# Optimization experiments

Measured on AMD Instinct MI355X. Metric: run time of the kernel, lower is better.

The kernel has to match this reference:

```python
import jax, jax.numpy as jnp
import numpy as np

N_NODES = 100000
N_EDGES = 3200000
D_IN = 256
D_OUT = 256


def setup_inputs() -> dict:
    key = jax.random.key(0)
    k1, k2, k3, k4, k5 = jax.random.split(key, 5)
    x = jax.random.normal(k1, (N_NODES, D_IN), dtype=jnp.float32)
    edge_val = jax.random.uniform(k2, (N_EDGES,), dtype=jnp.float32)
    weight = jax.random.normal(k3, (D_IN, D_OUT), dtype=jnp.float32)
    bias = jnp.zeros((D_OUT,), dtype=jnp.float32)
    edge_row = jax.random.randint(k4, (N_EDGES,), 0, N_NODES, dtype=jnp.int32)
    edge_col = jax.random.randint(k5, (N_EDGES,), 0, N_NODES, dtype=jnp.int32)
    return {"x": x, "edge_val": edge_val, "weight": weight, "bias": bias,
            "edge_row": edge_row, "edge_col": edge_col}


def reference(x, edge_val, weight, bias, edge_row, edge_col):
    # Dense feature transform: support = x @ W  -> [N, D_OUT]
    support = x @ weight
    # SpMM with COO adjacency: out[i] = sum_{e: row[e]=i} val[e] * support[col[e]]
    messages = edge_val[:, None] * support[edge_col]        # [E, D_OUT] gather
    out = jax.ops.segment_sum(messages, edge_row, num_segments=N_NODES)
    return out + bias
```

## Files before the change

kernel.cpp:

```cpp
#include <hip/hip_runtime.h>

#define D 256
#define BSHIFT 7
#define BROWS 128
#define CHUNK 8192

typedef __attribute__((ext_vector_type(8))) short bf16x8;
typedef __attribute__((ext_vector_type(4))) float f32x4;

__device__ inline ushort f2bf_rne(float f) {
    uint u = __builtin_bit_cast(uint, f);
    return (ushort)((u + 0x7FFFu + ((u >> 16) & 1u)) >> 16);
}

__global__ __launch_bounds__(256) void prep(const float* __restrict__ w,
                                            ushort* __restrict__ wt,
                                            int* __restrict__ bcnt, int NB) {
    const int idx = blockIdx.x * 256 + threadIdx.x;
    if (idx < D * D) {
        const int n = idx >> 8, k = idx & 255;
        wt[n * 256 + k] = f2bf_rne(w[k * 256 + n]);
    } else if (idx - D * D < NB) {
        bcnt[idx - D * D] = 0;
    }
}

__global__ __launch_bounds__(256) void bucket_hist(const int* __restrict__ edge_row,
                                                   int* __restrict__ bcnt,
                                                   int E, int NB) {
    __shared__ int bh[1024];
    const int tid = threadIdx.x;
    for (int i = tid; i < 1024; i += 256) bh[i] = 0;
    __syncthreads();

    const int e0 = blockIdx.x * CHUNK;
    const int e1 = min(e0 + CHUNK, E);
    for (int i = e0 + tid * 4; i < e1; i += 1024) {
        if (i + 3 < e1) {
            const int4 r = *(const int4*)(edge_row + i);
            atomicAdd(&bh[r.x >> BSHIFT], 1);
            atomicAdd(&bh[r.y >> BSHIFT], 1);
            atomicAdd(&bh[r.z >> BSHIFT], 1);
            atomicAdd(&bh[r.w >> BSHIFT], 1);
        } else {
            for (int j = i; j < e1; ++j) atomicAdd(&bh[edge_row[j] >> BSHIFT], 1);
        }
    }
    __syncthreads();

    for (int b = tid; b < NB; b += 256) {
        const int c = bh[b];
        if (c) atomicAdd(&bcnt[b], c);
    }
}

__global__ __launch_bounds__(512) void bucket_scan(const int* __restrict__ bcnt,
                                                   int* __restrict__ bstart,
                                                   int* __restrict__ bcursor,
                                                   int* __restrict__ row_start,
                                                   int NB, int N, int E) {
    __shared__ int psum[512];
    const int tid = threadIdx.x;
    int v[4];
    int s = 0;
#pragma unroll
    for (int k = 0; k < 4; ++k) {
        const int i = tid * 4 + k;
        v[k] = (i < NB) ? bcnt[i] : 0;
        s += v[k];
    }
    psum[tid] = s;
    __syncthreads();
#pragma unroll
    for (int off = 1; off < 512; off <<= 1) {
        const int t = (tid >= off) ? psum[tid - off] : 0;
        __syncthreads();
        psum[tid] += t;
        __syncthreads();
    }
    int run = psum[tid] - s;
#pragma unroll
    for (int k = 0; k < 4; ++k) {
        const int i = tid * 4 + k;
        if (i < NB) { bstart[i] = run; bcursor[i] = run; }
        run += v[k];
    }
    if (tid == 0) { bstart[NB] = E; row_start[N] = E; }
}

union SMemGS {
    ushort As[64 * 256];
    int    cur[1024];
};

__global__ __launch_bounds__(256) void gemm_scatter(
        const float* __restrict__ x, const ushort* __restrict__ wt,
        ushort* __restrict__ sup, int N, int ngemm,
        const int* __restrict__ edge_row, const int* __restrict__ edge_col,
        const float* __restrict__ edge_val, int* __restrict__ bcursor,
        unsigned long long* __restrict__ ebuck, int E, int NB, int nchunk) {
    __shared__ SMemGS sm;
    const int tid = threadIdx.x;
    const int bid = blockIdx.x;

    const bool is_scatter = ((bid % 5) == 4) && (bid / 5 < nchunk);

    if (!is_scatter) {
        const int gb = bid - (bid + 1) / 5;
        if (gb >= ngemm) return;
        const int wv  = tid >> 6;
        const int ln  = tid & 63;
        const int row0 = gb * 64;

        for (int i = tid; i < 64 * 64; i += 256) {
            const int r = i >> 6, c = i & 63;
            int gr = row0 + r;
            if (gr >= N) gr = N - 1;
            const float4 xv = *(const float4*)(x + (size_t)gr * D + c * 4);
            ushort4 b;
            b.x = f2bf_rne(xv.x); b.y = f2bf_rne(xv.y);
            b.z = f2bf_rne(xv.z); b.w = f2bf_rne(xv.w);
            const int byte = (r * 512 + c * 8) ^ ((r & 7) << 4);
            *(ushort4*)((char*)sm.As + byte) = b;
        }
        __syncthreads();

        f32x4 acc[16];
#pragma unroll
        for (int n = 0; n < 16; ++n) acc[n] = (f32x4){0.f, 0.f, 0.f, 0.f};

        const int arow = wv * 16 + (ln & 15);
        const int ksub = (ln >> 4) * 16;
        const ushort* wbase = wt + (ln & 15) * 256;

#pragma unroll
        for (int kk = 0; kk < 8; ++kk) {
            const int abyte = (arow * 512 + kk * 64 + ksub) ^ ((arow & 7) << 4);
            const bf16x8 af = *(const bf16x8*)((const char*)sm.As + abyte);
            const ushort* wp = wbase + kk * 32 + (ln >> 4) * 8;
#pragma unroll
            for (int n = 0; n < 16; ++n) {
                const bf16x8 bf = *(const bf16x8*)(wp + n * 16 * 256);
                acc[n] = __builtin_amdgcn_mfma_f32_16x16x32_bf16(af, bf, acc[n], 0, 0, 0);
            }
        }

        const int crow = row0 + wv * 16 + (ln >> 4) * 4;
        const int ccol = ln & 15;
#pragma unroll
        for (int n = 0; n < 16; ++n) {
#pragma unroll
            for (int reg = 0; reg < 4; ++reg) {
                const int r = crow + reg;
                if (r < N) sup[(size_t)r * D + n * 16 + ccol] = f2bf_rne(acc[n][reg]);
            }
        }
    } else {
        const int e0 = (bid / 5) * CHUNK;
        const int e1 = min(e0 + CHUNK, E);

        for (int i = tid; i < 1024; i += 256) sm.cur[i] = 0;
        __syncthreads();

        for (int e = e0 + tid; e < e1; e += 256)
            atomicAdd(&sm.cur[edge_row[e] >> BSHIFT], 1);
        __syncthreads();

        for (int b = tid; b < NB; b += 256) {
            const int c = sm.cur[b];
            sm.cur[b] = (c > 0) ? atomicAdd(&bcursor[b], c) : 0;
        }
        __syncthreads();

        for (int e = e0 + tid; e < e1; e += 256) {
            const int r = edge_row[e];
            const int b = r >> BSHIFT;
            const int pos = atomicAdd(&sm.cur[b], 1);
            const unsigned long long pk =
                ((unsigned long long)(uint)f2bf_rne(edge_val[e]) << 48) |
                ((unsigned long long)(uint)edge_col[e] << 17) | (uint)r;
            ebuck[pos] = pk;
        }
    }
}

__device__ inline long long pack_cv(int c, float v) {
    return (long long)(((unsigned long long)__builtin_bit_cast(uint, v) << 32) |
                       (uint)c);
}

__global__ __launch_bounds__(256) void fine_scatter(
        const unsigned long long* __restrict__ ebuck,
        const int* __restrict__ bstart,
        long long* __restrict__ epair,
        int* __restrict__ row_start, int N) {
    __shared__ int cnt[BROWS];
    __shared__ int cur[BROWS];
    const int tid = threadIdx.x;
    const int r0  = blockIdx.x << BSHIFT;
    const int s   = bstart[blockIdx.x];
    const int e   = bstart[blockIdx.x + 1];

    if (tid < BROWS) cnt[tid] = 0;
    __syncthreads();

    for (int i = s + tid; i < e; i += 256)
        atomicAdd(&cnt[(int)(ebuck[i] & 0x1FFFFu) - r0], 1);
    __syncthreads();

    if (tid < BROWS) cur[tid] = cnt[tid];
    __syncthreads();
#pragma unroll
    for (int off = 1; off < BROWS; off <<= 1) {
        const int t = (tid < BROWS && tid >= off) ? cur[tid - off] : 0;
        __syncthreads();
        if (tid < BROWS) cur[tid] += t;
        __syncthreads();
    }
    if (tid < BROWS) {
        const int rs = s + cur[tid] - cnt[tid];
        cur[tid] = rs;
        const int row = r0 + tid;
        if (row < N) row_start[row] = rs;
    }
    __syncthreads();

    for (int i = s + tid; i < e; i += 256) {
        const unsigned long long pk = ebuck[i];
        const int  r  = (int)(pk & 0x1FFFFu) - r0;
        const int  c  = (int)((pk >> 17) & 0x1FFFFu);
        const float v = __builtin_bit_cast(float, (uint)(pk >> 48) << 16);
        const int pos = atomicAdd(&cur[r], 1);
        epair[pos] = pack_cv(c, v);
    }
}

__global__ __launch_bounds__(256) void accumulate(const ushort* __restrict__ sup,
                                                  const int* __restrict__ row_start,
                                                  const long long* __restrict__ epair,
                                                  const float* __restrict__ bias,
                                                  float* __restrict__ out, int N) {
    const int row = blockIdx.x * 4 + (threadIdx.x >> 6);
    if (row >= N) return;
    const int lane = threadIdx.x & 63;
    const int lofs = lane * 4;

    const int s = row_start[row];
    const int e = row_start[row + 1];

    f32x4 a[8];
    a[0] = *(const f32x4*)(bias + lofs);
#pragma unroll
    for (int q = 1; q < 8; ++q) a[q] = (f32x4){0.f, 0.f, 0.f, 0.f};

    for (int base = s; base < e; base += 64) {
        const int idx = base + lane;
        long long pk = 0;
        if (idx < e) pk = __builtin_nontemporal_load(epair + idx);
        const int   c = (int)(uint)pk;
        const float v = __builtin_bit_cast(float, (uint)((unsigned long long)pk >> 32));
        const int n = min(64, e - base);
        int j = 0;
        for (; j + 15 < n; j += 16) {
            int   cq[16];
            float vq[16];
            uint2 uq[16];
#pragma unroll
            for (int q = 0; q < 16; ++q) {
                cq[q] = __shfl(c, j + q);
                vq[q] = __shfl(v, j + q);
            }
#pragma unroll
            for (int q = 0; q < 16; ++q)
                uq[q] = *(const uint2*)(sup + ((uint)cq[q] << 8) + lofs);
#pragma unroll
            for (int q = 0; q < 16; ++q) {
                const float f0 = __builtin_bit_cast(float, uq[q].x << 16);
                const float f1 = __builtin_bit_cast(float, uq[q].x & 0xFFFF0000u);
                const float f2 = __builtin_bit_cast(float, uq[q].y << 16);
                const float f3 = __builtin_bit_cast(float, uq[q].y & 0xFFFF0000u);
                a[q & 7][0] = fmaf(vq[q], f0, a[q & 7][0]);
                a[q & 7][1] = fmaf(vq[q], f1, a[q & 7][1]);
                a[q & 7][2] = fmaf(vq[q], f2, a[q & 7][2]);
                a[q & 7][3] = fmaf(vq[q], f3, a[q & 7][3]);
            }
        }
        for (; j + 7 < n; j += 8) {
            int   cq[8];
            float vq[8];
            uint2 uq[8];
#pragma unroll
            for (int q = 0; q < 8; ++q) {
                cq[q] = __shfl(c, j + q);
                vq[q] = __shfl(v, j + q);
            }
#pragma unroll
            for (int q = 0; q < 8; ++q)
                uq[q] = *(const uint2*)(sup + ((uint)cq[q] << 8) + lofs);
#pragma unroll
            for (int q = 0; q < 8; ++q) {
                const float f0 = __builtin_bit_cast(float, uq[q].x << 16);
                const float f1 = __builtin_bit_cast(float, uq[q].x & 0xFFFF0000u);
                const float f2 = __builtin_bit_cast(float, uq[q].y << 16);
                const float f3 = __builtin_bit_cast(float, uq[q].y & 0xFFFF0000u);
                a[q][0] = fmaf(vq[q], f0, a[q][0]);
                a[q][1] = fmaf(vq[q], f1, a[q][1]);
                a[q][2] = fmaf(vq[q], f2, a[q][2]);
                a[q][3] = fmaf(vq[q], f3, a[q][3]);
            }
        }
        for (; j < n; ++j) {
            const int   c0 = __shfl(c, j);
            const float v0 = __shfl(v, j);
            const uint2 u  = *(const uint2*)(sup + ((uint)c0 << 8) + lofs);
            const float f0 = __builtin_bit_cast(float, u.x << 16);
            const float f1 = __builtin_bit_cast(float, u.x & 0xFFFF0000u);
            const float f2 = __builtin_bit_cast(float, u.y << 16);
            const float f3 = __builtin_bit_cast(float, u.y & 0xFFFF0000u);
            a[0][0] = fmaf(v0, f0, a[0][0]);
            a[0][1] = fmaf(v0, f1, a[0][1]);
            a[0][2] = fmaf(v0, f2, a[0][2]);
            a[0][3] = fmaf(v0, f3, a[0][3]);
        }
    }
#pragma unroll
    for (int q = 1; q < 8; ++q) {
        a[0][0] += a[q][0]; a[0][1] += a[q][1];
        a[0][2] += a[q][2]; a[0][3] += a[q][3];
    }
    __builtin_nontemporal_store(a[0], (f32x4*)(out + (size_t)row * D + lofs));
}

extern "C" void kernel_launch(void* const* d_in, const int* in_sizes, int n_in,
                              void* d_out, int out_size, void* d_ws, size_t ws_size,
                              hipStream_t stream) {
    const float* x        = (const float*)d_in[0];
    const float* edge_val = (const float*)d_in[1];
    const float* weight   = (const float*)d_in[2];
    const float* bias     = (const float*)d_in[3];
    const int*   edge_row = (const int*)d_in[4];
    const int*   edge_col = (const int*)d_in[5];
    float*       out      = (float*)d_out;

    const int N = in_sizes[0] / D;
    const int E = in_sizes[1];

    char* ws = (char*)d_ws;
    size_t off = 0;
    auto carve = [&](size_t bytes) -> char* {
        char* p = ws + off;
        off = (off + bytes + 255) & ~(size_t)255;
        return p;
    };

    const int NB = (N + BROWS - 1) / BROWS;

    ushort* sup = (ushort*)carve((size_t)N * D * sizeof(ushort));
    ushort* wt  = (ushort*)carve((size_t)D * D * sizeof(ushort));
    unsigned long long* ebuck =
        (unsigned long long*)carve((size_t)E * sizeof(unsigned long long));
    long long* epair = (long long*)carve((size_t)E * sizeof(long long));
    int* row_start = (int*)carve((size_t)(N + 1) * sizeof(int));
    int* bcnt      = (int*)carve((size_t)NB * sizeof(int));
    int* bstart    = (int*)carve((size_t)(NB + 1) * sizeof(int));
    int* bcursor   = (int*)carve((size_t)NB * sizeof(int));

    const int ngemm  = (N + 63) / 64;
    const int nchunk = (E + CHUNK - 1) / CHUNK;
    const int ngrid = 5 * nchunk;

    prep<<<(D * D + NB + 255) / 256, 256, 0, stream>>>(weight, wt, bcnt, NB);

    bucket_hist<<<nchunk, 256, 0, stream>>>(edge_row, bcnt, E, NB);
    bucket_scan<<<1, 512, 0, stream>>>(bcnt, bstart, bcursor, row_start, NB, N, E);

    gemm_scatter<<<ngrid, 256, 0, stream>>>(
        x, wt, sup, N, ngemm, edge_row, edge_col, edge_val, bcursor, ebuck, E, NB,
        nchunk);

    fine_scatter<<<NB, 256, 0, stream>>>(ebuck, bstart, epair, row_start, N);

    accumulate<<<(N + 3) / 4, 256, 0, stream>>>(sup, row_start, epair, bias, out, N);
}
```

Measured before the change: 400.3 us.

## Fuse fine bucket sort with row accumulation and halve bucket size

The per-bucket fine scatter and the per-row gather-accumulate are merged into one kernel. Each block first sorts its bucket's edges by row in a scratch buffer, then its four waves accumulate that bucket's rows straight from the just-written pairs. Buckets shrink from 128 to 64 rows, doubling the histogram and scatter shared arrays, and the global row_start array plus one kernel launch go away. The intent is to cut a launch and keep the epair reads hot in cache. The cost is fewer, heavier blocks (one per 64 rows) with a barrier between the two phases, which may lower latency hiding and add load imbalance.

```diff
diff --git a/kernel.cpp b/kernel.cpp
--- a/kernel.cpp
+++ b/kernel.cpp
@@ -1,8 +1,8 @@
 #include <hip/hip_runtime.h>
 
 #define D 256
-#define BSHIFT 7
-#define BROWS 128
+#define BSHIFT 6
+#define BROWS 64
 #define CHUNK 8192
 
 typedef __attribute__((ext_vector_type(8))) short bf16x8;
@@ -28,9 +28,9 @@
 __global__ __launch_bounds__(256) void bucket_hist(const int* __restrict__ edge_row,
                                                    int* __restrict__ bcnt,
                                                    int E, int NB) {
-    __shared__ int bh[1024];
+    __shared__ int bh[2048];
     const int tid = threadIdx.x;
-    for (int i = tid; i < 1024; i += 256) bh[i] = 0;
+    for (int i = tid; i < 2048; i += 256) bh[i] = 0;
     __syncthreads();
 
     const int e0 = blockIdx.x * CHUNK;
@@ -57,8 +57,7 @@
 __global__ __launch_bounds__(512) void bucket_scan(const int* __restrict__ bcnt,
                                                    int* __restrict__ bstart,
                                                    int* __restrict__ bcursor,
-                                                   int* __restrict__ row_start,
-                                                   int NB, int N, int E) {
+                                                   int NB, int E) {
     __shared__ int psum[512];
     const int tid = threadIdx.x;
     int v[4];
@@ -85,12 +84,12 @@
         if (i < NB) { bstart[i] = run; bcursor[i] = run; }
         run += v[k];
     }
-    if (tid == 0) { bstart[NB] = E; row_start[N] = E; }
+    if (tid == 0) bstart[NB] = E;
 }
 
 union SMemGS {
     ushort As[64 * 256];
-    int    cur[1024];
+    int    cur[2048];
 };
 
 __global__ __launch_bounds__(256) void gemm_scatter(
@@ -159,7 +158,7 @@
         const int e0 = (bid / 5) * CHUNK;
         const int e1 = min(e0 + CHUNK, E);
 
-        for (int i = tid; i < 1024; i += 256) sm.cur[i] = 0;
+        for (int i = tid; i < 2048; i += 256) sm.cur[i] = 0;
         __syncthreads();
 
         for (int e = e0 + tid; e < e1; e += 256)
@@ -189,17 +188,23 @@
                        (uint)c);
 }
 
-__global__ __launch_bounds__(256) void fine_scatter(
+__global__ __launch_bounds__(256) void sort_accumulate(
+        const ushort* __restrict__ sup,
         const unsigned long long* __restrict__ ebuck,
         const int* __restrict__ bstart,
         long long* __restrict__ epair,
-        int* __restrict__ row_start, int N) {
+        const float* __restrict__ bias,
+        float* __restrict__ out, int N) {
     __shared__ int cnt[BROWS];
     __shared__ int cur[BROWS];
-    const int tid = threadIdx.x;
-    const int r0  = blockIdx.x << BSHIFT;
-    const int s   = bstart[blockIdx.x];
-    const int e   = bstart[blockIdx.x + 1];
+    __shared__ int srow[BROWS + 1];
+    const int tid  = threadIdx.x;
+    const int lane = tid & 63;
+    const int wv   = tid >> 6;
+    const int r0   = blockIdx.x << BSHIFT;
+    const int s    = bstart[blockIdx.x];
+    const int e    = bstart[blockIdx.x + 1];
+    const int lofs = lane * 4;
 
     if (tid < BROWS) cnt[tid] = 0;
     __syncthreads();
@@ -218,11 +223,11 @@
         __syncthreads();
     }
     if (tid < BROWS) {
-        const int rs = s + cur[tid] - cnt[tid];
-        cur[tid] = rs;
-        const int row = r0 + tid;
-        if (row < N) row_start[row] = rs;
-    }
+        const int ex = cur[tid] - cnt[tid];
+        srow[tid] = ex;
+        cur[tid]  = s + ex;
+    }
+    if (tid == 0) srow[BROWS] = e - s;
     __syncthreads();
 
     for (int i = s + tid; i < e; i += 256) {
@@ -233,102 +238,96 @@
         const int pos = atomicAdd(&cur[r], 1);
         epair[pos] = pack_cv(c, v);
     }
-}
-
-__global__ __launch_bounds__(256) void accumulate(const ushort* __restrict__ sup,
-                                                  const int* __restrict__ row_start,
-                                                  const long long* __restrict__ epair,
-                                                  const float* __restrict__ bias,
-                                                  float* __restrict__ out, int N) {
-    const int row = blockIdx.x * 4 + (threadIdx.x >> 6);
-    if (row >= N) return;
-    const int lane = threadIdx.x & 63;
-    const int lofs = lane * 4;
-
-    const int s = row_start[row];
-    const int e = row_start[row + 1];
-
-    f32x4 a[8];
-    a[0] = *(const f32x4*)(bias + lofs);
-#pragma unroll
-    for (int q = 1; q < 8; ++q) a[q] = (f32x4){0.f, 0.f, 0.f, 0.f};
-
-    for (int base = s; base < e; base += 64) {
-        const int idx = base + lane;
-        long long pk = 0;
-        if (idx < e) pk = __builtin_nontemporal_load(epair + idx);
-        const int   c = (int)(uint)pk;
-        const float v = __builtin_bit_cast(float, (uint)((unsigned long long)pk >> 32));
-        const int n = min(64, e - base);
-        int j = 0;
-        for (; j + 15 < n; j += 16) {
-            int   cq[16];
-            float vq[16];
-            uint2 uq[16];
-#pragma unroll
-            for (int q = 0; q < 16; ++q) {
-                cq[q] = __shfl(c, j + q);
-                vq[q] = __shfl(v, j + q);
-            }
-#pragma unroll
-            for (int q = 0; q < 16; ++q)
-                uq[q] = *(const uint2*)(sup + ((uint)cq[q] << 8) + lofs);
-#pragma unroll
-            for (int q = 0; q < 16; ++q) {
-                const float f0 = __builtin_bit_cast(float, uq[q].x << 16);
-                const float f1 = __builtin_bit_cast(float, uq[q].x & 0xFFFF0000u);
-                const float f2 = __builtin_bit_cast(float, uq[q].y << 16);
-                const float f3 = __builtin_bit_cast(float, uq[q].y & 0xFFFF0000u);
-                a[q & 7][0] = fmaf(vq[q], f0, a[q & 7][0]);
-                a[q & 7][1] = fmaf(vq[q], f1, a[q & 7][1]);
-                a[q & 7][2] = fmaf(vq[q], f2, a[q & 7][2]);
-                a[q & 7][3] = fmaf(vq[q], f3, a[q & 7][3]);
-            }
-        }
-        for (; j + 7 < n; j += 8) {
-            int   cq[8];
-            float vq[8];
-            uint2 uq[8];
-#pragma unroll
-            for (int q = 0; q < 8; ++q) {
-                cq[q] = __shfl(c, j + q);
-                vq[q] = __shfl(v, j + q);
-            }
-#pragma unroll
-            for (int q = 0; q < 8; ++q)
-                uq[q] = *(const uint2*)(sup + ((uint)cq[q] << 8) + lofs);
-#pragma unroll
-            for (int q = 0; q < 8; ++q) {
-                const float f0 = __builtin_bit_cast(float, uq[q].x << 16);
-                const float f1 = __builtin_bit_cast(float, uq[q].x & 0xFFFF0000u);
-                const float f2 = __builtin_bit_cast(float, uq[q].y << 16);
-                const float f3 = __builtin_bit_cast(float, uq[q].y & 0xFFFF0000u);
-                a[q][0] = fmaf(vq[q], f0, a[q][0]);
-                a[q][1] = fmaf(vq[q], f1, a[q][1]);
-                a[q][2] = fmaf(vq[q], f2, a[q][2]);
-                a[q][3] = fmaf(vq[q], f3, a[q][3]);
-            }
-        }
-        for (; j < n; ++j) {
-            const int   c0 = __shfl(c, j);
-            const float v0 = __shfl(v, j);
-            const uint2 u  = *(const uint2*)(sup + ((uint)c0 << 8) + lofs);
-            const float f0 = __builtin_bit_cast(float, u.x << 16);
-            const float f1 = __builtin_bit_cast(float, u.x & 0xFFFF0000u);
-            const float f2 = __builtin_bit_cast(float, u.y << 16);
-            const float f3 = __builtin_bit_cast(float, u.y & 0xFFFF0000u);
-            a[0][0] = fmaf(v0, f0, a[0][0]);
-            a[0][1] = fmaf(v0, f1, a[0][1]);
-            a[0][2] = fmaf(v0, f2, a[0][2]);
-            a[0][3] = fmaf(v0, f3, a[0][3]);
-        }
-    }
-#pragma unroll
-    for (int q = 1; q < 8; ++q) {
-        a[0][0] += a[q][0]; a[0][1] += a[q][1];
-        a[0][2] += a[q][2]; a[0][3] += a[q][3];
-    }
-    __builtin_nontemporal_store(a[0], (f32x4*)(out + (size_t)row * D + lofs));
+    __syncthreads();
+
+    for (int r = wv; r < BROWS; r += 4) {
+        const int row = r0 + r;
+        if (row >= N) break;
+        const int rs = s + srow[r];
+        const int re = s + srow[r + 1];
+
+        f32x4 a[8];
+        a[0] = *(const f32x4*)(bias + lofs);
+#pragma unroll
+        for (int q = 1; q < 8; ++q) a[q] = (f32x4){0.f, 0.f, 0.f, 0.f};
+
+        for (int base = rs; base < re; base += 64) {
+            const int idx = base + lane;
+            long long pk = 0;
+            if (idx < re) pk = epair[idx];
+            const int   c = (int)(uint)pk;
+            const float v = __builtin_bit_cast(float, (uint)((unsigned long long)pk >> 32));
+            const int n = min(64, re - base);
+            int j = 0;
+            for (; j + 15 < n; j += 16) {
+                int   cq[16];
+                float vq[16];
+                uint2 uq[16];
+#pragma unroll
+                for (int q = 0; q < 16; ++q) {
+                    cq[q] = __shfl(c, j + q);
+                    vq[q] = __shfl(v, j + q);
+                }
+#pragma unroll
+                for (int q = 0; q < 16; ++q)
+                    uq[q] = *(const uint2*)(sup + ((uint)cq[q] << 8) + lofs);
+#pragma unroll
+                for (int q = 0; q < 16; ++q) {
+                    const float f0 = __builtin_bit_cast(float, uq[q].x << 16);
+                    const float f1 = __builtin_bit_cast(float, uq[q].x & 0xFFFF0000u);
+                    const float f2 = __builtin_bit_cast(float, uq[q].y << 16);
+                    const float f3 = __builtin_bit_cast(float, uq[q].y & 0xFFFF0000u);
+                    a[q & 7][0] = fmaf(vq[q], f0, a[q & 7][0]);
+                    a[q & 7][1] = fmaf(vq[q], f1, a[q & 7][1]);
+                    a[q & 7][2] = fmaf(vq[q], f2, a[q & 7][2]);
+                    a[q & 7][3] = fmaf(vq[q], f3, a[q & 7][3]);
+                }
+            }
+            for (; j + 7 < n; j += 8) {
+                int   cq[8];
+                float vq[8];
+                uint2 uq[8];
+#pragma unroll
+                for (int q = 0; q < 8; ++q) {
+                    cq[q] = __shfl(c, j + q);
+                    vq[q] = __shfl(v, j + q);
+                }
+#pragma unroll
+                for (int q = 0; q < 8; ++q)
+                    uq[q] = *(const uint2*)(sup + ((uint)cq[q] << 8) + lofs);
+#pragma unroll
+                for (int q = 0; q < 8; ++q) {
+                    const float f0 = __builtin_bit_cast(float, uq[q].x << 16);
+                    const float f1 = __builtin_bit_cast(float, uq[q].x & 0xFFFF0000u);
+                    const float f2 = __builtin_bit_cast(float, uq[q].y << 16);
+                    const float f3 = __builtin_bit_cast(float, uq[q].y & 0xFFFF0000u);
+                    a[q][0] = fmaf(vq[q], f0, a[q][0]);
+                    a[q][1] = fmaf(vq[q], f1, a[q][1]);
+                    a[q][2] = fmaf(vq[q], f2, a[q][2]);
+                    a[q][3] = fmaf(vq[q], f3, a[q][3]);
+                }
+            }
+            for (; j < n; ++j) {
+                const int   c0 = __shfl(c, j);
+                const float v0 = __shfl(v, j);
+                const uint2 u  = *(const uint2*)(sup + ((uint)c0 << 8) + lofs);
+                const float f0 = __builtin_bit_cast(float, u.x << 16);
+                const float f1 = __builtin_bit_cast(float, u.x & 0xFFFF0000u);
+                const float f2 = __builtin_bit_cast(float, u.y << 16);
+                const float f3 = __builtin_bit_cast(float, u.y & 0xFFFF0000u);
+                a[0][0] = fmaf(v0, f0, a[0][0]);
+                a[0][1] = fmaf(v0, f1, a[0][1]);
+                a[0][2] = fmaf(v0, f2, a[0][2]);
+                a[0][3] = fmaf(v0, f3, a[0][3]);
+            }
+        }
+#pragma unroll
+        for (int q = 1; q < 8; ++q) {
+            a[0][0] += a[q][0]; a[0][1] += a[q][1];
+            a[0][2] += a[q][2]; a[0][3] += a[q][3];
+        }
+        __builtin_nontemporal_store(a[0], (f32x4*)(out + (size_t)row * D + lofs));
+    }
 }
 
 extern "C" void kernel_launch(void* const* d_in, const int* in_sizes, int n_in,
@@ -360,25 +359,22 @@
     unsigned long long* ebuck =
         (unsigned long long*)carve((size_t)E * sizeof(unsigned long long));
     long long* epair = (long long*)carve((size_t)E * sizeof(long long));
-    int* row_start = (int*)carve((size_t)(N + 1) * sizeof(int));
-    int* bcnt      = (int*)carve((size_t)NB * sizeof(int));
-    int* bstart    = (int*)carve((size_t)(NB + 1) * sizeof(int));
-    int* bcursor   = (int*)carve((size_t)NB * sizeof(int));
+    int* bcnt    = (int*)carve((size_t)NB * sizeof(int));
+    int* bstart  = (int*)carve((size_t)(NB + 1) * sizeof(int));
+    int* bcursor = (int*)carve((size_t)NB * sizeof(int));
 
     const int ngemm  = (N + 63) / 64;
     const int nchunk = (E + CHUNK - 1) / CHUNK;
-    const int ngrid = 5 * nchunk;
+    const int ngrid  = 5 * nchunk;
 
     prep<<<(D * D + NB + 255) / 256, 256, 0, stream>>>(weight, wt, bcnt, NB);
 
     bucket_hist<<<nchunk, 256, 0, stream>>>(edge_row, bcnt, E, NB);
-    bucket_scan<<<1, 512, 0, stream>>>(bcnt, bstart, bcursor, row_start, NB, N, E);
+    bucket_scan<<<1, 512, 0, stream>>>(bcnt, bstart, bcursor, NB, E);
 
     gemm_scatter<<<ngrid, 256, 0, stream>>>(
         x, wt, sup, N, ngemm, edge_row, edge_col, edge_val, bcursor, ebuck, E, NB,
         nchunk);
 
-    fine_scatter<<<NB, 256, 0, stream>>>(ebuck, bstart, epair, row_start, N);
-
-    accumulate<<<(N + 3) / 4, 256, 0, stream>>>(sup, row_start, epair, bias, out, N);
-}
+    sort_accumulate<<<NB, 256, 0, stream>>>(sup, ebuck, bstart, epair, bias, out, N);
+}
```

Measured after the change: 419.3 us. +4.7%, slower.
